# Kernel optimization log

Hardware: AMD Instinct MI355X
Metric: run time of the kernel (lower is better)

The kernel has to match this reference:

```python
import jax, jax.numpy as jnp
import numpy as np

N = 50000       # nodes
E = 800000      # edges
D_IN = 128
D_OUT = 128
K = 3           # num_stacks
T = 2           # num_layers


def setup_inputs() -> dict:
    key = jax.random.key(0)
    ks = jax.random.split(key, 10)
    feats = jax.random.normal(ks[0], (N, D_IN), dtype=jnp.float32)
    src = jax.random.randint(ks[1], (E,), 0, N, dtype=jnp.int32)
    dst = jax.random.randint(ks[2], (E,), 0, N, dtype=jnp.int32)
    s = 0.05
    w0 = jax.random.normal(ks[3], (K, D_IN, D_OUT), dtype=jnp.float32) * s
    b0 = jax.random.normal(ks[4], (K, D_OUT), dtype=jnp.float32) * s
    w = jax.random.normal(ks[5], (K, D_OUT, D_OUT), dtype=jnp.float32) * s
    bw = jax.random.normal(ks[6], (K, D_OUT), dtype=jnp.float32) * s
    v = jax.random.normal(ks[7], (K, D_IN, D_OUT), dtype=jnp.float32) * s
    bv = jax.random.normal(ks[8], (K, D_OUT), dtype=jnp.float32) * s
    return {"feats": feats, "src": src, "dst": dst,
            "w0": w0, "b0": b0, "w": w, "bw": bw, "v": v, "bv": bv}


def _propagate(h, src, dst, norm):
    # symmetric degree-normalized SpMM: D^{-1/2} A D^{-1/2} h
    h = h * norm                                   # [N, d]
    agg = jax.ops.segment_sum(h[src], dst, num_segments=N)  # gather + scatter-add
    return agg * norm


def reference(feats, src, dst, w0, b0, w, bw, v, bv):
    ones = jnp.ones((E,), dtype=feats.dtype)
    deg = jnp.clip(jax.ops.segment_sum(ones, dst, num_segments=N), 1.0)
    norm = (deg ** -0.5)[:, None]                  # [N, 1]

    out = jnp.zeros((N, D_OUT), dtype=feats.dtype)
    for k in range(K):
        h = feats
        for t in range(T):
            h = _propagate(h, src, dst, norm)
            if t == 0:
                h = h @ w0[k] + b0[k]
            else:
                h = h @ w[k] + bw[k]
            h = h + (feats @ v[k] + bv[k])         # dropout is identity (p=0, eval)
            h = jax.nn.relu(h)
        out = out + h
    return out / K
```

## Files before the change

kernel.cpp:

```cpp
#include <hip/hip_runtime.h>

#define N_NODES 50000
#define N_EDGES 800000
#define D 128
#define PLANE ((size_t)N_NODES * D)
#define NCHUNK ((N_NODES + 255) / 256)

typedef float f32x4 __attribute__((ext_vector_type(4)));
typedef float f32x2 __attribute__((ext_vector_type(2)));
typedef short bf16x8 __attribute__((ext_vector_type(8)));

__device__ __forceinline__ unsigned short f2bf(float x) {
  unsigned int u = __float_as_uint(x);
  u += 0x7FFFu + ((u >> 16) & 1u);
  return (unsigned short)(u >> 16);
}
__device__ __forceinline__ float bf2f(unsigned short h) {
  return __uint_as_float((unsigned int)h << 16);
}
__device__ __forceinline__ unsigned char f32_to_fp8(float x) {
  int p = __builtin_amdgcn_cvt_pk_fp8_f32(x, x, 0, false);
  return (unsigned char)(p & 0xFF);
}
__device__ __forceinline__ void fp8x4_to_f32(int pk, float* f) {
  f32x2 lo = __builtin_amdgcn_cvt_pk_f32_fp8(pk, false);
  f32x2 hi = __builtin_amdgcn_cvt_pk_f32_fp8(pk, true);
  f[0] = lo.x; f[1] = lo.y; f[2] = hi.x; f[3] = hi.y;
}


__global__ __launch_bounds__(256) void scan_local(const int* __restrict__ cnt,
                                                  int* __restrict__ local,
                                                  int* __restrict__ partial) {
  __shared__ int s[256];
  int t = threadIdx.x;
  int i = blockIdx.x * 256 + t;
  int v = (i < N_NODES) ? cnt[i] : 0;
  s[t] = v;
  __syncthreads();
  for (int off = 1; off < 256; off <<= 1) {
    int tmp = (t >= off) ? s[t - off] : 0;
    __syncthreads();
    s[t] += tmp;
    __syncthreads();
  }
  if (i < N_NODES) local[i] = s[t] - v;
  if (t == 255) partial[blockIdx.x] = s[255];
}

__global__ __launch_bounds__(256) void scan_chunks(const int* __restrict__ partial,
                                                   int* __restrict__ chunk_off,
                                                   int* __restrict__ rowptr) {
  __shared__ int s[256];
  int t = threadIdx.x;
  int v = (t < NCHUNK) ? partial[t] : 0;
  s[t] = v;
  __syncthreads();
  for (int off = 1; off < 256; off <<= 1) {
    int tmp = (t >= off) ? s[t - off] : 0;
    __syncthreads();
    s[t] += tmp;
    __syncthreads();
  }
  if (t < NCHUNK) chunk_off[t] = s[t] - v;
  if (t == 255) rowptr[N_NODES] = s[255];
}

__global__ __launch_bounds__(256) void finalize_rows(const int* __restrict__ cnt,
                                                     const int* __restrict__ local,
                                                     const int* __restrict__ chunk_off,
                                                     int* __restrict__ rowptr,
                                                     int* __restrict__ cursor,
                                                     float* __restrict__ norm) {
  int i = blockIdx.x * 256 + threadIdx.x;
  if (i < N_NODES) {
    int r = local[i] + chunk_off[blockIdx.x];
    rowptr[i] = r;
    cursor[i] = r;
    int d = cnt[i];
    if (d < 1) d = 1;
    norm[i] = rsqrtf((float)d);
  }
}

__global__ __launch_bounds__(256) void fill_csr(const int* __restrict__ src,
                                                const int* __restrict__ dst,
                                                int* __restrict__ cursor,
                                                int* __restrict__ col) {
  int e = blockIdx.x * blockDim.x + threadIdx.x;
  if (e < N_EDGES) {
    int pos = atomicAdd(&cursor[dst[e]], 1);
    col[pos] = src[e];
  }
}


#define CONV_THREADS ((int)(PLANE / 4))
#define WT_THREADS (2 * 3 * 128 * 256)
#define PREP_TOTAL (CONV_THREADS + WT_THREADS + N_EDGES)

__global__ __launch_bounds__(256) void prep_all(const float* __restrict__ feats,
                                                const float* __restrict__ w0,
                                                const float* __restrict__ w,
                                                const float* __restrict__ v,
                                                const int* __restrict__ dst,
                                                unsigned short* __restrict__ feats_bf,
                                                unsigned char* __restrict__ feats_fp8,
                                                unsigned short* __restrict__ bt_h1,
                                                unsigned short* __restrict__ bt_out,
                                                int* __restrict__ cnt) {
  int idx = blockIdx.x * 256 + threadIdx.x;
  if (idx < CONV_THREADS) {
    float4 x = ((const float4*)feats)[idx];
    ushort4 o;
    o.x = f2bf(x.x);
    o.y = f2bf(x.y);
    o.z = f2bf(x.z);
    o.w = f2bf(x.w);
    ((ushort4*)feats_bf)[idx] = o;
    int p = __builtin_amdgcn_cvt_pk_fp8_f32(x.x, x.y, 0, false);
    p = __builtin_amdgcn_cvt_pk_fp8_f32(x.z, x.w, p, true);
    ((int*)feats_fp8)[idx] = p;
    return;
  }
  idx -= CONV_THREADS;
  if (idx < WT_THREADS) {
    int buf = idx / 98304;
    int rem = idx - buf * 98304;
    int stack = rem / 32768;
    int rem2 = rem & 32767;
    int n = rem2 >> 8;
    int k = rem2 & 255;
    const float* srcm;
    int kk;
    if (k < 128) {
      srcm = (buf == 0) ? w0 : w;
      kk = k;
    } else {
      srcm = v;
      kk = k - 128;
    }
    float val = srcm[(size_t)stack * 16384 + (size_t)kk * 128 + n];
    unsigned short* dstb = (buf == 0) ? bt_h1 : bt_out;
    dstb[(size_t)stack * 32768 + (size_t)n * 256 + k] = f2bf(val);
    return;
  }
  idx -= WT_THREADS;
  if (idx < N_EDGES) atomicAdd(&cnt[dst[idx]], 1);
}


template <int NK>
__global__ __launch_bounds__(256) void spmm_fp8(const unsigned char* __restrict__ h,
                                                const float* __restrict__ norm,
                                                const int* __restrict__ rowptr,
                                                const int* __restrict__ col,
                                                unsigned short* __restrict__ out) {
  int row = blockIdx.x * 4 + (threadIdx.x >> 6);
  if (row >= N_NODES) return;
  int lane = threadIdx.x & 63;
  int sub = lane >> 3;
  int c8 = lane & 7;
  int beg = rowptr[row], end = rowptr[row + 1];

  float acc[NK][16];
#pragma unroll
  for (int m = 0; m < NK; ++m)
#pragma unroll
    for (int j = 0; j < 16; ++j) acc[m][j] = 0.f;

#pragma unroll 2
  for (int e = beg; e < end; e += 8) {
    int eidx = e + sub;
    bool valid = eidx < end;
    int s = valid ? col[eidx] : 0;
    float wgt = valid ? norm[s] : 0.f;
    const unsigned char* hp = h + (size_t)s * D + c8 * 16;
#pragma unroll
    for (int m = 0; m < NK; ++m) {
      int4 pkt = *(const int4*)(hp + m * PLANE);
      float f[16];
      fp8x4_to_f32(pkt.x, f + 0);
      fp8x4_to_f32(pkt.y, f + 4);
      fp8x4_to_f32(pkt.z, f + 8);
      fp8x4_to_f32(pkt.w, f + 12);
#pragma unroll
      for (int j = 0; j < 16; ++j) acc[m][j] = fmaf(wgt, f[j], acc[m][j]);
    }
  }

#pragma unroll
  for (int m = 0; m < NK; ++m)
#pragma unroll
    for (int j = 0; j < 16; ++j) {
      float vv = acc[m][j];
      vv += __shfl_xor(vv, 8);
      vv += __shfl_xor(vv, 16);
      vv += __shfl_xor(vv, 32);
      acc[m][j] = vv;
    }

  if (sub == 0) {
    float nd = norm[row];
#pragma unroll
    for (int m = 0; m < NK; ++m) {
      bf16x8 o0, o1;
#pragma unroll
      for (int j = 0; j < 8; ++j) {
        o0[j] = (short)f2bf(acc[m][j] * nd);
        o1[j] = (short)f2bf(acc[m][j + 8] * nd);
      }
      unsigned short* op = out + m * PLANE + (size_t)row * D + c8 * 16;
      *(bf16x8*)op = o0;
      *(bf16x8*)(op + 8) = o1;
    }
  }
}


__device__ __forceinline__ void stage_B64(unsigned short (*Bs)[256],
                                          const unsigned short* __restrict__ Btg,
                                          int nh, int tid) {
#pragma unroll
  for (int i = 0; i < 8; ++i) {
    int t = tid + i * 256;
    int n = t >> 5;
    int kc = t & 31;
    int kcs = kc ^ (n & 31);
    *(bf16x8*)&Bs[n][kcs * 8] = *(const bf16x8*)(Btg + (size_t)(nh + n) * 256 + kc * 8);
  }
}

__device__ __forceinline__ bf16x8 read_B64(const unsigned short (*Bs)[256], int n,
                                           int chunk) {
  return *(const bf16x8*)&Bs[n][(chunk ^ (n & 31)) * 8];
}

__global__ __launch_bounds__(256) void gemm_h1_fused(
    const unsigned short* __restrict__ P,
    const unsigned short* __restrict__ feats_bf,
    const unsigned short* __restrict__ Bt,
    const float* __restrict__ b0, const float* __restrict__ bv,
    unsigned char* __restrict__ h1_fp8) {
  __shared__ unsigned short Bs[64][256];
  int nh = blockIdx.y * 64;

  int tid = threadIdx.x;
  int lane = tid & 63;
  int wv = tid >> 6;
  int ln15 = lane & 15;
  int g = lane >> 4;

  int m0 = blockIdx.x * 128 + wv * 32;
  int r0 = m0 + ln15;
  int r1 = m0 + 16 + ln15;
  if (r0 >= N_NODES) r0 = N_NODES - 1;
  if (r1 >= N_NODES) r1 = N_NODES - 1;

  bf16x8 a0[8], a1[8];
#pragma unroll
  for (int s = 0; s < 4; ++s) {
    a0[s] = *(const bf16x8*)(P + (size_t)r0 * 128 + g * 8 + s * 32);
    a1[s] = *(const bf16x8*)(P + (size_t)r1 * 128 + g * 8 + s * 32);
    a0[s + 4] = *(const bf16x8*)(feats_bf + (size_t)r0 * 128 + g * 8 + s * 32);
    a1[s + 4] = *(const bf16x8*)(feats_bf + (size_t)r1 * 128 + g * 8 + s * 32);
  }

  for (int stk = 0; stk < 3; ++stk) {
    if (stk) __syncthreads();
    stage_B64(Bs, Bt + (size_t)stk * 32768, nh, tid);
    __syncthreads();

    f32x4 acc0[4], acc1[4];
#pragma unroll
    for (int nt = 0; nt < 4; ++nt) { acc0[nt] = (f32x4)(0.f); acc1[nt] = (f32x4)(0.f); }

#pragma unroll
    for (int s = 0; s < 8; ++s) {
#pragma unroll
      for (int nt = 0; nt < 4; ++nt) {
        bf16x8 bfr = read_B64(Bs, nt * 16 + ln15, s * 4 + g);
        acc0[nt] = __builtin_amdgcn_mfma_f32_16x16x32_bf16(a0[s], bfr, acc0[nt], 0, 0, 0);
        acc1[nt] = __builtin_amdgcn_mfma_f32_16x16x32_bf16(a1[s], bfr, acc1[nt], 0, 0, 0);
      }
    }

    unsigned char* outp = h1_fp8 + (size_t)stk * PLANE;
#pragma unroll
    for (int nt = 0; nt < 4; ++nt) {
      int colj = nh + nt * 16 + ln15;
      float bsum = b0[stk * 128 + colj] + bv[stk * 128 + colj];
#pragma unroll
      for (int r = 0; r < 4; ++r) {
        int mA = m0 + g * 4 + r;
        int mB = m0 + 16 + g * 4 + r;
        if (mA < N_NODES) {
          float x = acc0[nt][r] + bsum;
          outp[(size_t)mA * 128 + colj] = f32_to_fp8(x > 0.f ? x : 0.f);
        }
        if (mB < N_NODES) {
          float x = acc1[nt][r] + bsum;
          outp[(size_t)mB * 128 + colj] = f32_to_fp8(x > 0.f ? x : 0.f);
        }
      }
    }
  }
}

__global__ __launch_bounds__(256) void gemm_out_fused(
    const unsigned short* __restrict__ agg,
    const unsigned short* __restrict__ feats_bf,
    const unsigned short* __restrict__ Bt,
    const float* __restrict__ bwp, const float* __restrict__ bvp,
    float* __restrict__ outp) {
  __shared__ unsigned short Bs[64][256];
  int nh = blockIdx.y * 64;

  int tid = threadIdx.x;
  int lane = tid & 63;
  int wv = tid >> 6;
  int ln15 = lane & 15;
  int g = lane >> 4;

  int m0 = blockIdx.x * 128 + wv * 32;
  int r0 = m0 + ln15;
  int r1 = m0 + 16 + ln15;
  if (r0 >= N_NODES) r0 = N_NODES - 1;
  if (r1 >= N_NODES) r1 = N_NODES - 1;

  bf16x8 f0[4], f1[4];
#pragma unroll
  for (int s = 0; s < 4; ++s) {
    f0[s] = *(const bf16x8*)(feats_bf + (size_t)r0 * 128 + g * 8 + s * 32);
    f1[s] = *(const bf16x8*)(feats_bf + (size_t)r1 * 128 + g * 8 + s * 32);
  }

  f32x4 sum0[4], sum1[4];
#pragma unroll
  for (int nt = 0; nt < 4; ++nt) { sum0[nt] = (f32x4)(0.f); sum1[nt] = (f32x4)(0.f); }

  for (int stk = 0; stk < 3; ++stk) {
    if (stk) __syncthreads();
    stage_B64(Bs, Bt + (size_t)stk * 32768, nh, tid);
    __syncthreads();

    const unsigned short* A1 = agg + (size_t)stk * PLANE;
    bf16x8 g0[4], g1[4];
#pragma unroll
    for (int s = 0; s < 4; ++s) {
      g0[s] = *(const bf16x8*)(A1 + (size_t)r0 * 128 + g * 8 + s * 32);
      g1[s] = *(const bf16x8*)(A1 + (size_t)r1 * 128 + g * 8 + s * 32);
    }

    f32x4 acc0[4], acc1[4];
#pragma unroll
    for (int nt = 0; nt < 4; ++nt) { acc0[nt] = (f32x4)(0.f); acc1[nt] = (f32x4)(0.f); }

#pragma unroll
    for (int s = 0; s < 8; ++s) {
      bf16x8 af0 = (s < 4) ? g0[s & 3] : f0[s & 3];
      bf16x8 af1 = (s < 4) ? g1[s & 3] : f1[s & 3];
#pragma unroll
      for (int nt = 0; nt < 4; ++nt) {
        bf16x8 bfr = read_B64(Bs, nt * 16 + ln15, s * 4 + g);
        acc0[nt] = __builtin_amdgcn_mfma_f32_16x16x32_bf16(af0, bfr, acc0[nt], 0, 0, 0);
        acc1[nt] = __builtin_amdgcn_mfma_f32_16x16x32_bf16(af1, bfr, acc1[nt], 0, 0, 0);
      }
    }

#pragma unroll
    for (int nt = 0; nt < 4; ++nt) {
      int colj = nh + nt * 16 + ln15;
      float bsum = bwp[stk * 128 + colj] + bvp[stk * 128 + colj];
#pragma unroll
      for (int r = 0; r < 4; ++r) {
        float x0 = acc0[nt][r] + bsum;
        float x1 = acc1[nt][r] + bsum;
        sum0[nt][r] += (x0 > 0.f ? x0 : 0.f);
        sum1[nt][r] += (x1 > 0.f ? x1 : 0.f);
      }
    }
  }

  const float sc = 1.0f / 3.0f;
#pragma unroll
  for (int nt = 0; nt < 4; ++nt) {
    int colj = nh + nt * 16 + ln15;
#pragma unroll
    for (int r = 0; r < 4; ++r) {
      int mA = m0 + g * 4 + r;
      int mB = m0 + 16 + g * 4 + r;
      if (mA < N_NODES) outp[(size_t)mA * 128 + colj] = sum0[nt][r] * sc;
      if (mB < N_NODES) outp[(size_t)mB * 128 + colj] = sum1[nt][r] * sc;
    }
  }
}


extern "C" void kernel_launch(void* const* d_in, const int* in_sizes, int n_in,
                              void* d_out, int out_size, void* d_ws, size_t ws_size,
                              hipStream_t stream) {
  const float* feats = (const float*)d_in[0];
  const int* src = (const int*)d_in[1];
  const int* dst = (const int*)d_in[2];
  const float* w0 = (const float*)d_in[3];
  const float* b0 = (const float*)d_in[4];
  const float* w = (const float*)d_in[5];
  const float* bw = (const float*)d_in[6];
  const float* v = (const float*)d_in[7];
  const float* bv = (const float*)d_in[8];
  float* out = (float*)d_out;

  char* ws = (char*)d_ws;
  size_t off = 0;
  auto alloc = [&](size_t bytes) {
    void* p = ws + off;
    off += (bytes + 255) & ~(size_t)255;
    return p;
  };
  int* cnt = (int*)alloc(N_NODES * 4);
  int* local = (int*)alloc(N_NODES * 4);
  int* partial = (int*)alloc(NCHUNK * 4);
  int* chunk_off = (int*)alloc(NCHUNK * 4);
  float* norm = (float*)alloc(N_NODES * 4);
  int* rowptr = (int*)alloc((N_NODES + 1) * 4);
  int* cursor = (int*)alloc(N_NODES * 4);
  int* col = (int*)alloc(N_EDGES * 4);
  unsigned short* bt_h1 = (unsigned short*)alloc(3 * 32768 * 2);
  unsigned short* bt_out = (unsigned short*)alloc(3 * 32768 * 2);

  size_t pb = PLANE * 2;
  unsigned short* feats_bf = (unsigned short*)alloc(pb);
  unsigned char* feats_fp8 = (unsigned char*)alloc(PLANE);
  unsigned short* P_bf = (unsigned short*)alloc(pb);
  unsigned char* h1_fp8 = (unsigned char*)alloc(3 * PLANE);
  unsigned short* agg_bf = (unsigned short*)alloc(3 * pb);

  hipMemsetAsync(cnt, 0, N_NODES * 4, stream);

  dim3 blk(256);
  prep_all<<<(PREP_TOTAL + 255) / 256, blk, 0, stream>>>(feats, w0, w, v, dst, feats_bf,
                                                         feats_fp8, bt_h1, bt_out, cnt);
  scan_local<<<NCHUNK, blk, 0, stream>>>(cnt, local, partial);
  scan_chunks<<<1, blk, 0, stream>>>(partial, chunk_off, rowptr);
  finalize_rows<<<NCHUNK, blk, 0, stream>>>(cnt, local, chunk_off, rowptr, cursor, norm);
  fill_csr<<<(N_EDGES + 255) / 256, blk, 0, stream>>>(src, dst, cursor, col);

  int sblocks = (N_NODES + 3) / 4;
  int mblocks = (N_NODES + 127) / 128;
  dim3 ggrid(mblocks, 2);

  spmm_fp8<1><<<sblocks, blk, 0, stream>>>(feats_fp8, norm, rowptr, col, P_bf);
  gemm_h1_fused<<<ggrid, blk, 0, stream>>>(P_bf, feats_bf, bt_h1, b0, bv, h1_fp8);
  spmm_fp8<3><<<sblocks, blk, 0, stream>>>(h1_fp8, norm, rowptr, col, agg_bf);
  gemm_out_fused<<<ggrid, blk, 0, stream>>>(agg_bf, feats_bf, bt_out, bw, bv, out);
}
```

Measured before the change: 350.4 us.

## Pre-scale fp8 features by norm, interleave stacks, degree-sort rows for SpMM

The source-side degree normalization is now folded into the fp8 features when they are produced (in the conversion pass and in the gemm_h1 epilogue), which removes the per-edge norm gather in SpMM. The three h1 stacks are stored interleaved per node with a 384-byte stride, so one gathered row brings in all three stacks. SpMM now gives each row to 8 lanes and walks its edges serially with packed fp8-to-f32 adds, dropping the cross-lane shuffle reduction. Rows are visited through a degree-bucketed permutation so waves get balanced work. The cost is extra histogram/permutation work in the CSR build and less coalescing, since lanes in a wave now gather different rows.

```diff
diff --git a/kernel.cpp b/kernel.cpp
--- a/kernel.cpp
+++ b/kernel.cpp
@@ -15,29 +15,25 @@
   u += 0x7FFFu + ((u >> 16) & 1u);
   return (unsigned short)(u >> 16);
 }
-__device__ __forceinline__ float bf2f(unsigned short h) {
-  return __uint_as_float((unsigned int)h << 16);
-}
 __device__ __forceinline__ unsigned char f32_to_fp8(float x) {
   int p = __builtin_amdgcn_cvt_pk_fp8_f32(x, x, 0, false);
   return (unsigned char)(p & 0xFF);
 }
-__device__ __forceinline__ void fp8x4_to_f32(int pk, float* f) {
-  f32x2 lo = __builtin_amdgcn_cvt_pk_f32_fp8(pk, false);
-  f32x2 hi = __builtin_amdgcn_cvt_pk_f32_fp8(pk, true);
-  f[0] = lo.x; f[1] = lo.y; f[2] = hi.x; f[3] = hi.y;
-}
 
 
 __global__ __launch_bounds__(256) void scan_local(const int* __restrict__ cnt,
                                                   int* __restrict__ local,
-                                                  int* __restrict__ partial) {
+                                                  int* __restrict__ partial,
+                                                  int* __restrict__ bcnt) {
   __shared__ int s[256];
+  __shared__ int hist[64];
   int t = threadIdx.x;
+  if (t < 64) hist[t] = 0;
   int i = blockIdx.x * 256 + t;
   int v = (i < N_NODES) ? cnt[i] : 0;
   s[t] = v;
   __syncthreads();
+  if (i < N_NODES) atomicAdd(&hist[v < 63 ? v : 63], 1);
   for (int off = 1; off < 256; off <<= 1) {
     int tmp = (t >= off) ? s[t - off] : 0;
     __syncthreads();
@@ -46,16 +42,26 @@
   }
   if (i < N_NODES) local[i] = s[t] - v;
   if (t == 255) partial[blockIdx.x] = s[255];
+  if (t < 64) atomicAdd(&bcnt[t], hist[t]);
 }
 
 __global__ __launch_bounds__(256) void scan_chunks(const int* __restrict__ partial,
                                                    int* __restrict__ chunk_off,
-                                                   int* __restrict__ rowptr) {
+                                                   int* __restrict__ rowptr,
+                                                   const int* __restrict__ bcnt,
+                                                   int* __restrict__ gcur) {
   __shared__ int s[256];
+  __shared__ int sb[64];
+  __shared__ int sbb[64];
   int t = threadIdx.x;
   int v = (t < NCHUNK) ? partial[t] : 0;
   s[t] = v;
+  if (t < 64) sb[t] = bcnt[t];
   __syncthreads();
+  if (t == 0) {
+    int run = 0;
+    for (int q = 0; q < 64; ++q) { sbb[q] = run; run += sb[q]; }
+  }
   for (int off = 1; off < 256; off <<= 1) {
     int tmp = (t >= off) ? s[t - off] : 0;
     __syncthreads();
@@ -64,6 +70,7 @@
   }
   if (t < NCHUNK) chunk_off[t] = s[t] - v;
   if (t == 255) rowptr[N_NODES] = s[255];
+  if (t < 64) gcur[t] = sbb[t];
 }
 
 __global__ __launch_bounds__(256) void finalize_rows(const int* __restrict__ cnt,
@@ -71,26 +78,35 @@
                                                      const int* __restrict__ chunk_off,
                                                      int* __restrict__ rowptr,
                                                      int* __restrict__ cursor,
-                                                     float* __restrict__ norm) {
-  int i = blockIdx.x * 256 + threadIdx.x;
+                                                     float* __restrict__ norm,
+                                                     int* __restrict__ gcur,
+                                                     int* __restrict__ perm) {
+  __shared__ int hcnt[64];
+  __shared__ int hbase[64];
+  int t = threadIdx.x;
+  if (t < 64) hcnt[t] = 0;
+  __syncthreads();
+  int i = blockIdx.x * 256 + t;
+  int b = 0;
   if (i < N_NODES) {
     int r = local[i] + chunk_off[blockIdx.x];
     rowptr[i] = r;
     cursor[i] = r;
     int d = cnt[i];
+    b = d < 63 ? d : 63;
+    atomicAdd(&hcnt[b], 1);
     if (d < 1) d = 1;
     norm[i] = rsqrtf((float)d);
   }
-}
-
-__global__ __launch_bounds__(256) void fill_csr(const int* __restrict__ src,
-                                                const int* __restrict__ dst,
-                                                int* __restrict__ cursor,
-                                                int* __restrict__ col) {
-  int e = blockIdx.x * blockDim.x + threadIdx.x;
-  if (e < N_EDGES) {
-    int pos = atomicAdd(&cursor[dst[e]], 1);
-    col[pos] = src[e];
+  __syncthreads();
+  if (t < 64) {
+    hbase[t] = atomicAdd(&gcur[t], hcnt[t]);
+    hcnt[t] = 0;
+  }
+  __syncthreads();
+  if (i < N_NODES) {
+    int lp = atomicAdd(&hcnt[b], 1);
+    perm[hbase[b] + lp] = i;
   }
 }
 
@@ -105,7 +121,6 @@
                                                 const float* __restrict__ v,
                                                 const int* __restrict__ dst,
                                                 unsigned short* __restrict__ feats_bf,
-                                                unsigned char* __restrict__ feats_fp8,
                                                 unsigned short* __restrict__ bt_h1,
                                                 unsigned short* __restrict__ bt_out,
                                                 int* __restrict__ cnt) {
@@ -118,9 +133,6 @@
     o.z = f2bf(x.z);
     o.w = f2bf(x.w);
     ((ushort4*)feats_bf)[idx] = o;
-    int p = __builtin_amdgcn_cvt_pk_fp8_f32(x.x, x.y, 0, false);
-    p = __builtin_amdgcn_cvt_pk_fp8_f32(x.z, x.w, p, true);
-    ((int*)feats_fp8)[idx] = p;
     return;
   }
   idx -= CONV_THREADS;
@@ -149,71 +161,81 @@
   if (idx < N_EDGES) atomicAdd(&cnt[dst[idx]], 1);
 }
 
-
-template <int NK>
-__global__ __launch_bounds__(256) void spmm_fp8(const unsigned char* __restrict__ h,
-                                                const float* __restrict__ norm,
-                                                const int* __restrict__ rowptr,
-                                                const int* __restrict__ col,
-                                                unsigned short* __restrict__ out) {
-  int row = blockIdx.x * 4 + (threadIdx.x >> 6);
-  if (row >= N_NODES) return;
-  int lane = threadIdx.x & 63;
-  int sub = lane >> 3;
-  int c8 = lane & 7;
+__global__ __launch_bounds__(256) void csr_fp8(const int* __restrict__ src,
+                                               const int* __restrict__ dst,
+                                               int* __restrict__ cursor,
+                                               int* __restrict__ col,
+                                               const float* __restrict__ feats,
+                                               const float* __restrict__ norm,
+                                               unsigned char* __restrict__ feats_fp8) {
+  int idx = blockIdx.x * 256 + threadIdx.x;
+  if (idx < CONV_THREADS) {
+    float4 x = ((const float4*)feats)[idx];
+    float nv = norm[idx >> 5];
+    int p = __builtin_amdgcn_cvt_pk_fp8_f32(x.x * nv, x.y * nv, 0, false);
+    p = __builtin_amdgcn_cvt_pk_fp8_f32(x.z * nv, x.w * nv, p, true);
+    ((int*)feats_fp8)[idx] = p;
+    return;
+  }
+  idx -= CONV_THREADS;
+  if (idx < N_EDGES) {
+    int pos = atomicAdd(&cursor[dst[idx]], 1);
+    col[pos] = src[idx];
+  }
+}
+
+
+template <int NK, int STRIDE>
+__global__ __launch_bounds__(256) void spmm_rows(const unsigned char* __restrict__ h,
+                                                 const float* __restrict__ norm,
+                                                 const int* __restrict__ rowptr,
+                                                 const int* __restrict__ col,
+                                                 const int* __restrict__ perm,
+                                                 unsigned short* __restrict__ out) {
+  int gi = blockIdx.x * 32 + (threadIdx.x >> 3);
+  if (gi >= N_NODES) return;
+  int l = threadIdx.x & 7;
+  int row = perm[gi];
   int beg = rowptr[row], end = rowptr[row + 1];
 
-  float acc[NK][16];
+  f32x2 acc[NK][8];
 #pragma unroll
   for (int m = 0; m < NK; ++m)
 #pragma unroll
-    for (int j = 0; j < 16; ++j) acc[m][j] = 0.f;
+    for (int j = 0; j < 8; ++j) acc[m][j] = (f32x2)(0.f);
 
 #pragma unroll 2
-  for (int e = beg; e < end; e += 8) {
-    int eidx = e + sub;
-    bool valid = eidx < end;
-    int s = valid ? col[eidx] : 0;
-    float wgt = valid ? norm[s] : 0.f;
-    const unsigned char* hp = h + (size_t)s * D + c8 * 16;
+  for (int e = beg; e < end; ++e) {
+    int s = col[e];
+    const unsigned char* hp = h + (size_t)s * STRIDE + l * 16;
 #pragma unroll
     for (int m = 0; m < NK; ++m) {
-      int4 pkt = *(const int4*)(hp + m * PLANE);
-      float f[16];
-      fp8x4_to_f32(pkt.x, f + 0);
-      fp8x4_to_f32(pkt.y, f + 4);
-      fp8x4_to_f32(pkt.z, f + 8);
-      fp8x4_to_f32(pkt.w, f + 12);
-#pragma unroll
-      for (int j = 0; j < 16; ++j) acc[m][j] = fmaf(wgt, f[j], acc[m][j]);
-    }
-  }
-
-#pragma unroll
-  for (int m = 0; m < NK; ++m)
-#pragma unroll
-    for (int j = 0; j < 16; ++j) {
-      float vv = acc[m][j];
-      vv += __shfl_xor(vv, 8);
-      vv += __shfl_xor(vv, 16);
-      vv += __shfl_xor(vv, 32);
-      acc[m][j] = vv;
-    }
-
-  if (sub == 0) {
-    float nd = norm[row];
-#pragma unroll
-    for (int m = 0; m < NK; ++m) {
-      bf16x8 o0, o1;
-#pragma unroll
-      for (int j = 0; j < 8; ++j) {
-        o0[j] = (short)f2bf(acc[m][j] * nd);
-        o1[j] = (short)f2bf(acc[m][j + 8] * nd);
-      }
-      unsigned short* op = out + m * PLANE + (size_t)row * D + c8 * 16;
-      *(bf16x8*)op = o0;
-      *(bf16x8*)(op + 8) = o1;
-    }
+      int4 p = *(const int4*)(hp + m * 128);
+      acc[m][0] += __builtin_amdgcn_cvt_pk_f32_fp8(p.x, false);
+      acc[m][1] += __builtin_amdgcn_cvt_pk_f32_fp8(p.x, true);
+      acc[m][2] += __builtin_amdgcn_cvt_pk_f32_fp8(p.y, false);
+      acc[m][3] += __builtin_amdgcn_cvt_pk_f32_fp8(p.y, true);
+      acc[m][4] += __builtin_amdgcn_cvt_pk_f32_fp8(p.z, false);
+      acc[m][5] += __builtin_amdgcn_cvt_pk_f32_fp8(p.z, true);
+      acc[m][6] += __builtin_amdgcn_cvt_pk_f32_fp8(p.w, false);
+      acc[m][7] += __builtin_amdgcn_cvt_pk_f32_fp8(p.w, true);
+    }
+  }
+
+  float nd = norm[row];
+#pragma unroll
+  for (int m = 0; m < NK; ++m) {
+    bf16x8 o0, o1;
+#pragma unroll
+    for (int j = 0; j < 4; ++j) {
+      o0[2 * j] = (short)f2bf(acc[m][j].x * nd);
+      o0[2 * j + 1] = (short)f2bf(acc[m][j].y * nd);
+      o1[2 * j] = (short)f2bf(acc[m][j + 4].x * nd);
+      o1[2 * j + 1] = (short)f2bf(acc[m][j + 4].y * nd);
+    }
+    unsigned short* op = out + (size_t)m * PLANE + (size_t)row * D + l * 16;
+    *(bf16x8*)op = o0;
+    *(bf16x8*)(op + 8) = o1;
   }
 }
 
@@ -241,6 +263,7 @@
     const unsigned short* __restrict__ feats_bf,
     const unsigned short* __restrict__ Bt,
     const float* __restrict__ b0, const float* __restrict__ bv,
+    const float* __restrict__ norm,
     unsigned char* __restrict__ h1_fp8) {
   __shared__ unsigned short Bs[64][256];
   int nh = blockIdx.y * 64;
@@ -266,6 +289,15 @@
     a1[s + 4] = *(const bf16x8*)(feats_bf + (size_t)r1 * 128 + g * 8 + s * 32);
   }
 
+  float nA[4], nB[4];
+#pragma unroll
+  for (int r = 0; r < 4; ++r) {
+    int mA = m0 + g * 4 + r;
+    int mB = m0 + 16 + g * 4 + r;
+    nA[r] = (mA < N_NODES) ? norm[mA] : 0.f;
+    nB[r] = (mB < N_NODES) ? norm[mB] : 0.f;
+  }
+
   for (int stk = 0; stk < 3; ++stk) {
     if (stk) __syncthreads();
     stage_B64(Bs, Bt + (size_t)stk * 32768, nh, tid);
@@ -285,7 +317,6 @@
       }
     }
 
-    unsigned char* outp = h1_fp8 + (size_t)stk * PLANE;
 #pragma unroll
     for (int nt = 0; nt < 4; ++nt) {
       int colj = nh + nt * 16 + ln15;
@@ -296,11 +327,13 @@
         int mB = m0 + 16 + g * 4 + r;
         if (mA < N_NODES) {
           float x = acc0[nt][r] + bsum;
-          outp[(size_t)mA * 128 + colj] = f32_to_fp8(x > 0.f ? x : 0.f);
+          x = x > 0.f ? x : 0.f;
+          h1_fp8[(size_t)mA * 384 + stk * 128 + colj] = f32_to_fp8(x * nA[r]);
         }
         if (mB < N_NODES) {
           float x = acc1[nt][r] + bsum;
-          outp[(size_t)mB * 128 + colj] = f32_to_fp8(x > 0.f ? x : 0.f);
+          x = x > 0.f ? x : 0.f;
+          h1_fp8[(size_t)mB * 384 + stk * 128 + colj] = f32_to_fp8(x * nB[r]);
         }
       }
     }
@@ -418,7 +451,9 @@
     off += (bytes + 255) & ~(size_t)255;
     return p;
   };
-  int* cnt = (int*)alloc(N_NODES * 4);
+  int* cnt = (int*)alloc((N_NODES + 128) * 4);
+  int* bcnt = cnt + N_NODES;
+  int* gcur = bcnt + 64;
   int* local = (int*)alloc(N_NODES * 4);
   int* partial = (int*)alloc(NCHUNK * 4);
   int* chunk_off = (int*)alloc(NCHUNK * 4);
@@ -426,6 +461,7 @@
   int* rowptr = (int*)alloc((N_NODES + 1) * 4);
   int* cursor = (int*)alloc(N_NODES * 4);
   int* col = (int*)alloc(N_EDGES * 4);
+  int* perm = (int*)alloc(N_NODES * 4);
   unsigned short* bt_h1 = (unsigned short*)alloc(3 * 32768 * 2);
   unsigned short* bt_out = (unsigned short*)alloc(3 * 32768 * 2);
 
@@ -436,22 +472,24 @@
   unsigned char* h1_fp8 = (unsigned char*)alloc(3 * PLANE);
   unsigned short* agg_bf = (unsigned short*)alloc(3 * pb);
 
-  hipMemsetAsync(cnt, 0, N_NODES * 4, stream);
+  hipMemsetAsync(cnt, 0, (N_NODES + 128) * 4, stream);
 
   dim3 blk(256);
   prep_all<<<(PREP_TOTAL + 255) / 256, blk, 0, stream>>>(feats, w0, w, v, dst, feats_bf,
-                                                         feats_fp8, bt_h1, bt_out, cnt);
-  scan_local<<<NCHUNK, blk, 0, stream>>>(cnt, local, partial);
-  scan_chunks<<<1, blk, 0, stream>>>(partial, chunk_off, rowptr);
-  finalize_rows<<<NCHUNK, blk, 0, stream>>>(cnt, local, chunk_off, rowptr, cursor, norm);
-  fill_csr<<<(N_EDGES + 255) / 256, blk, 0, stream>>>(src, dst, cursor, col);
-
-  int sblocks = (N_NODES + 3) / 4;
+                                                         bt_h1, bt_out, cnt);
+  scan_local<<<NCHUNK, blk, 0, stream>>>(cnt, local, partial, bcnt);
+  scan_chunks<<<1, blk, 0, stream>>>(partial, chunk_off, rowptr, bcnt, gcur);
+  finalize_rows<<<NCHUNK, blk, 0, stream>>>(cnt, local, chunk_off, rowptr, cursor, norm,
+                                            gcur, perm);
+  csr_fp8<<<(CONV_THREADS + N_EDGES + 255) / 256, blk, 0, stream>>>(
+      src, dst, cursor, col, feats, norm, feats_fp8);
+
+  int sblocks = (N_NODES + 31) / 32;
   int mblocks = (N_NODES + 127) / 128;
   dim3 ggrid(mblocks, 2);
 
-  spmm_fp8<1><<<sblocks, blk, 0, stream>>>(feats_fp8, norm, rowptr, col, P_bf);
-  gemm_h1_fused<<<ggrid, blk, 0, stream>>>(P_bf, feats_bf, bt_h1, b0, bv, h1_fp8);
-  spmm_fp8<3><<<sblocks, blk, 0, stream>>>(h1_fp8, norm, rowptr, col, agg_bf);
+  spmm_rows<1, 128><<<sblocks, blk, 0, stream>>>(feats_fp8, norm, rowptr, col, perm, P_bf);
+  gemm_h1_fused<<<ggrid, blk, 0, stream>>>(P_bf, feats_bf, bt_h1, b0, bv, norm, h1_fp8);
+  spmm_rows<3, 384><<<sblocks, blk, 0, stream>>>(h1_fp8, norm, rowptr, col, perm, agg_bf);
   gemm_out_fused<<<ggrid, blk, 0, stream>>>(agg_bf, feats_bf, bt_out, bw, bv, out);
 }
```

Result: faster. 342.5 us (-2.3%).
